# Kernel optimization log

Measured on AMD Instinct MI355X. Metric: run time of the kernel, lower is better.

The kernel has to match this reference:

```python
import jax, jax.numpy as jnp
import numpy as np

N, E = 50000, 800000
IN_DIM, HID, OUT = 64, 128, 64
EPS = 1e-5  # BatchNorm eps


def setup_inputs() -> dict:
    key = jax.random.key(0)
    ks = jax.random.split(key, 16)
    def w(k, i, o):
        return jax.random.normal(k, (i, o), jnp.float32) / np.float32(np.sqrt(i))
    def bn(k):
        km, kv = jax.random.split(k)
        return (jnp.ones((HID,), jnp.float32),                       # gamma
                jnp.zeros((HID,), jnp.float32),                      # beta
                0.1 * jax.random.normal(km, (HID,), jnp.float32),    # running mean
                0.5 + jax.random.uniform(kv, (HID,), jnp.float32))   # running var
    g0, be0, m0, v0 = bn(ks[6])
    g1, be1, m1, v1 = bn(ks[7])
    g2, be2, m2, v2 = bn(ks[8])
    return {
        "x":   jax.random.normal(ks[0], (N, IN_DIM), jnp.float32),
        "src": jax.random.randint(ks[1], (E,), 0, N, jnp.int32),
        "dst": jax.random.randint(ks[2], (E,), 0, N, jnp.int32),
        "W0": w(ks[3], IN_DIM, HID), "b0": jnp.zeros((HID,), jnp.float32),
        "g0": g0, "be0": be0, "m0": m0, "v0": v0,
        "W1": w(ks[4], HID, HID), "b1": jnp.zeros((HID,), jnp.float32),
        "g1": g1, "be1": be1, "m1": m1, "v1": v1,
        "W2": w(ks[5], HID, HID), "b2": jnp.zeros((HID,), jnp.float32),
        "g2": g2, "be2": be2, "m2": m2, "v2": v2,
        "Wm1": w(ks[9], HID, HID), "bm1": jnp.zeros((HID,), jnp.float32),
        "Wm2": w(ks[10], HID, OUT), "bm2": jnp.zeros((OUT,), jnp.float32),
    }


def gcn_conv(x, src, dst, W, b):
    # PyG GCNConv: h = x @ W; add self loops; symmetric normalization; scatter-add; + bias
    h = x @ W                                                     # [N, F]
    ones = jnp.ones((src.shape[0],), h.dtype)
    deg = 1.0 + jax.ops.segment_sum(ones, dst, num_segments=N)   # self loop adds 1
    dinv = jax.lax.rsqrt(deg)                                     # deg^-1/2 (deg >= 1)
    coef = (dinv[src] * dinv[dst])[:, None]                       # per-edge norm
    agg = jax.ops.segment_sum(h[src] * coef, dst, num_segments=N)
    return agg + h * (dinv * dinv)[:, None] + b                   # self-loop term + bias


def bn_relu(x, g, be, m, v):
    # eval-mode BatchNorm1d followed by ReLU (dropout is identity in eval)
    return jax.nn.relu((x - m) * jax.lax.rsqrt(v + EPS) * g + be)


def reference(x, src, dst,
              W0, b0, g0, be0, m0, v0,
              W1, b1, g1, be1, m1, v1,
              W2, b2, g2, be2, m2, v2,
              Wm1, bm1, Wm2, bm2):
    h = bn_relu(gcn_conv(x, src, dst, W0, b0), g0, be0, m0, v0)
    h = bn_relu(gcn_conv(h, src, dst, W1, b1), g1, be1, m1, v1)
    h = bn_relu(gcn_conv(h, src, dst, W2, b2), g2, be2, m2, v2)
    h = jax.nn.relu(h @ Wm1 + bm1)
    return h @ Wm2 + bm2
```

## Files before the change

### kernel.cpp

```cpp
#include <hip/hip_runtime.h>
#include <hip/hip_fp16.h>

#define BN_EPS 1e-5f
#define BK 512
#define NBMAX 128
#define ECH 8192

typedef _Float16 half_t;
typedef _Float16 half8 __attribute__((ext_vector_type(8)));
typedef float floatx4 __attribute__((ext_vector_type(4)));


__global__ void hist_kernel(const int* __restrict__ dst, int* __restrict__ cnt, int E) {
  int e = blockIdx.x * blockDim.x + threadIdx.x;
  if (e < E) atomicAdd(&cnt[dst[e]], 1);
}

__global__ __launch_bounds__(256) void block_sum_kernel(
    const int* __restrict__ cnt, int* __restrict__ bsum, int n) {
  int base = blockIdx.x * 1024 + threadIdx.x * 4;
  int s = 0;
#pragma unroll
  for (int j = 0; j < 4; ++j) {
    int i = base + j;
    if (i < n) s += cnt[i];
  }
#pragma unroll
  for (int o = 32; o > 0; o >>= 1) s += __shfl_down(s, o);
  __shared__ int ws[4];
  int lane = threadIdx.x & 63, w = threadIdx.x >> 6;
  if (lane == 0) ws[w] = s;
  __syncthreads();
  if (threadIdx.x == 0) bsum[blockIdx.x] = ws[0] + ws[1] + ws[2] + ws[3];
}

__global__ void scan_sums_kernel(int* __restrict__ bsum, int nb) {
  int lane = threadIdx.x;
  int v = (lane < nb) ? bsum[lane] : 0;
  int orig = v;
#pragma unroll
  for (int o = 1; o < 64; o <<= 1) {
    int t = __shfl_up(v, o);
    if (lane >= o) v += t;
  }
  if (lane < nb) bsum[lane] = v - orig;
}

__global__ __launch_bounds__(256) void scan_apply_kernel(
    const int* __restrict__ cnt, const int* __restrict__ bsum,
    int* __restrict__ off, float* __restrict__ dinv, int n, int E) {
  __shared__ int ts[256];
  const int t = threadIdx.x;
  const int base = blockIdx.x * 1024 + t * 4;
  int c[4];
  int s = 0;
#pragma unroll
  for (int j = 0; j < 4; ++j) {
    int i = base + j;
    c[j] = (i < n) ? cnt[i] : 0;
    s += c[j];
  }
  ts[t] = s;
  __syncthreads();
  for (int o = 1; o < 256; o <<= 1) {
    int v = (t >= o) ? ts[t - o] : 0;
    __syncthreads();
    ts[t] += v;
    __syncthreads();
  }
  int prefix = bsum[blockIdx.x] + ((t == 0) ? 0 : ts[t - 1]);
#pragma unroll
  for (int j = 0; j < 4; ++j) {
    int i = base + j;
    if (i < n) {
      off[i] = prefix;
      dinv[i] = rsqrtf(1.0f + (float)c[j]);
      prefix += c[j];
    }
  }
  if (blockIdx.x == 0 && t == 0) off[n] = E;
}

__global__ __launch_bounds__(256) void bucket_hist_kernel(
    const int* __restrict__ dst, int* __restrict__ bcnt, int E, int nb) {
  __shared__ int h[NBMAX];
  const int t = threadIdx.x;
  for (int i = t; i < nb; i += 256) h[i] = 0;
  __syncthreads();
  const int base = blockIdx.x * ECH;
#pragma unroll 8
  for (int p = 0; p < ECH / 256; ++p) {
    int e = base + p * 256 + t;
    if (e < E) atomicAdd(&h[dst[e] >> 9], 1);
  }
  __syncthreads();
  for (int i = t; i < nb; i += 256)
    if (h[i]) atomicAdd(&bcnt[i], h[i]);
}

__global__ __launch_bounds__(128) void bucket_scan_kernel(
    const int* __restrict__ bcnt, int* __restrict__ bbase,
    int* __restrict__ bcursor, int nb, int E) {
  __shared__ int ts[128];
  const int t = threadIdx.x;
  int v = (t < nb) ? bcnt[t] : 0;
  ts[t] = v;
  __syncthreads();
  for (int o = 1; o < 128; o <<= 1) {
    int u = (t >= o) ? ts[t - o] : 0;
    __syncthreads();
    ts[t] += u;
    __syncthreads();
  }
  int excl = ts[t] - v;
  if (t < nb) { bbase[t] = excl; bcursor[t] = excl; }
  if (t == 0) bbase[nb] = E;
}

__global__ __launch_bounds__(256) void bucket_scatter_kernel(
    const int* __restrict__ src, const int* __restrict__ dst,
    int* __restrict__ bcursor, int2* __restrict__ tmp, int E, int nb) {
  __shared__ int h[NBMAX];
  const int t = threadIdx.x;
  for (int i = t; i < nb; i += 256) h[i] = 0;
  __syncthreads();
  const int base = blockIdx.x * ECH;
#pragma unroll 8
  for (int p = 0; p < ECH / 256; ++p) {
    int e = base + p * 256 + t;
    if (e < E) atomicAdd(&h[dst[e] >> 9], 1);
  }
  __syncthreads();
  for (int i = t; i < nb; i += 256) {
    int c = h[i];
    h[i] = c ? atomicAdd(&bcursor[i], c) : 0;
  }
  __syncthreads();
#pragma unroll 8
  for (int p = 0; p < ECH / 256; ++p) {
    int e = base + p * 256 + t;
    if (e < E) {
      int s = src[e], d = dst[e];
      int pos = atomicAdd(&h[d >> 9], 1);
      tmp[pos] = make_int2(s, d);
    }
  }
}

__global__ __launch_bounds__(256) void final_scatter_kernel(
    const int2* __restrict__ tmp, const int* __restrict__ bbase,
    const int* __restrict__ off, int* __restrict__ esrc, int n) {
  __shared__ int cur[BK];
  const int t = threadIdx.x;
  const int b = blockIdx.x;
  const int nbase = b * BK;
  const int nn = min(BK, n - nbase);
  for (int i = t; i < nn; i += 256) cur[i] = off[nbase + i];
  __syncthreads();
  const int e0 = bbase[b], e1 = bbase[b + 1];
  for (int e = e0 + t; e < e1; e += 256) {
    int2 r = tmp[e];
    int pos = atomicAdd(&cur[r.y - nbase], 1);
    esrc[pos] = r.x;
  }
}

__global__ void cvt_fp16_kernel(const float* __restrict__ in, __half* __restrict__ out,
                                int n4) {
  int i = blockIdx.x * blockDim.x + threadIdx.x;
  if (i >= n4) return;
  float4 v = *(const float4*)(in + (size_t)i * 4);
  union { __half h[4]; float2 f; } u;
  u.h[0] = __float2half_rn(v.x);
  u.h[1] = __float2half_rn(v.y);
  u.h[2] = __float2half_rn(v.z);
  u.h[3] = __float2half_rn(v.w);
  *(float2*)(out + (size_t)i * 4) = u.f;
}


template <int FIN, int FOUT, int EPI, bool HALFOUT>
__global__ __launch_bounds__(256) void mgemm_kernel(
    const __half* __restrict__ X, const float* __restrict__ W,
    const float* __restrict__ bias, const float* __restrict__ gam,
    const float* __restrict__ bet, const float* __restrict__ mean,
    const float* __restrict__ var, void* __restrict__ Yv, int n) {
  constexpr int LDK = 72;
  constexpr int NCI = FOUT / 16;
  __shared__ half_t Asm[128 * LDK];
  __shared__ half_t Bsm[FOUT * LDK];

  const int t = threadIdx.x;
  const int wave = t >> 6, lane = t & 63;
  const int quad = lane >> 4, l16 = lane & 15;
  const int rowBase = blockIdx.x * 128;

  floatx4 acc[2][NCI];
#pragma unroll
  for (int i = 0; i < 2; ++i)
#pragma unroll
    for (int ci = 0; ci < NCI; ++ci) acc[i][ci] = (floatx4){0.f, 0.f, 0.f, 0.f};

  for (int kc = 0; kc < FIN; kc += 64) {
    __syncthreads();
    {
      const int kq = t & 15, m0 = t >> 4;
#pragma unroll
      for (int p = 0; p < 8; ++p) {
        int m = p * 16 + m0;
        int row = rowBase + m;
        uint2 v = make_uint2(0u, 0u);
        if (row < n) v = *(const uint2*)(X + (size_t)row * FIN + kc + kq * 4);
        *(uint2*)&Asm[m * LDK + kq * 4] = v;
      }
    }
    {
#pragma unroll
      for (int c0 = 0; c0 < FOUT * 16; c0 += 256) {
        int c = c0 + t;
        int nn = c % FOUT;
        int kg = (c / FOUT) * 4;
        const float* wp = W + (size_t)(kc + kg) * FOUT + nn;
        half_t* d = &Bsm[nn * LDK + kg];
        d[0] = (half_t)wp[0];
        d[1] = (half_t)wp[FOUT];
        d[2] = (half_t)wp[2 * FOUT];
        d[3] = (half_t)wp[3 * FOUT];
      }
    }
    __syncthreads();
#pragma unroll
    for (int kk = 0; kk < 2; ++kk) {
      half8 a0 = *(const half8*)&Asm[(wave * 32 + l16) * LDK + kk * 32 + quad * 8];
      half8 a1 = *(const half8*)&Asm[(wave * 32 + 16 + l16) * LDK + kk * 32 + quad * 8];
#pragma unroll
      for (int ci = 0; ci < NCI; ++ci) {
        half8 b = *(const half8*)&Bsm[(ci * 16 + l16) * LDK + kk * 32 + quad * 8];
        acc[0][ci] = __builtin_amdgcn_mfma_f32_16x16x32_f16(a0, b, acc[0][ci], 0, 0, 0);
        acc[1][ci] = __builtin_amdgcn_mfma_f32_16x16x32_f16(a1, b, acc[1][ci], 0, 0, 0);
      }
    }
  }

  float sc[NCI], sh[NCI];
#pragma unroll
  for (int ci = 0; ci < NCI; ++ci) {
    int col = ci * 16 + l16;
    if constexpr (EPI == 3) {
      float s = gam[col] * rsqrtf(var[col] + BN_EPS);
      sc[ci] = s;
      sh[ci] = (bias[col] - mean[col]) * s + bet[col];
    } else if constexpr (EPI == 1 || EPI == 2) {
      sc[ci] = 1.f;
      sh[ci] = bias[col];
    } else {
      sc[ci] = 1.f;
      sh[ci] = 0.f;
    }
  }
#pragma unroll
  for (int ri = 0; ri < 2; ++ri)
#pragma unroll
    for (int ci = 0; ci < NCI; ++ci) {
      int col = ci * 16 + l16;
#pragma unroll
      for (int r = 0; r < 4; ++r) {
        int row = rowBase + wave * 32 + ri * 16 + quad * 4 + r;
        if (row < n) {
          float v = acc[ri][ci][r];
          if constexpr (EPI != 0) v = fmaf(v, sc[ci], sh[ci]);
          if constexpr (EPI == 1 || EPI == 3) v = fmaxf(v, 0.f);
          if constexpr (HALFOUT)
            ((half_t*)Yv)[(size_t)row * FOUT + col] = (half_t)v;
          else
            ((float*)Yv)[(size_t)row * FOUT + col] = v;
        }
      }
    }
}


__global__ __launch_bounds__(256) void agg64_kernel(
    const __half* __restrict__ h, const int* __restrict__ off,
    const int* __restrict__ esrc, const float* __restrict__ dinv,
    __half* __restrict__ out, int n) {
  int gi = blockIdx.x * 4 + (threadIdx.x >> 6);
  if (gi >= n) return;
  const int lane = threadIdx.x & 63;
  const float di = dinv[gi];

  float a = 0.f;
  int e = off[gi];
  const int e1 = off[gi + 1];
  for (; e + 4 <= e1; e += 4) {
    int s0 = esrc[e], s1 = esrc[e + 1], s2 = esrc[e + 2], s3 = esrc[e + 3];
    float h0 = __half2float(h[((size_t)s0 << 6) + lane]);
    float h1 = __half2float(h[((size_t)s1 << 6) + lane]);
    float h2 = __half2float(h[((size_t)s2 << 6) + lane]);
    float h3 = __half2float(h[((size_t)s3 << 6) + lane]);
    a = fmaf(dinv[s0] * di, h0, a);
    a = fmaf(dinv[s1] * di, h1, a);
    a = fmaf(dinv[s2] * di, h2, a);
    a = fmaf(dinv[s3] * di, h3, a);
  }
  for (; e < e1; ++e) {
    int s = esrc[e];
    a = fmaf(dinv[s] * di, __half2float(h[((size_t)s << 6) + lane]), a);
  }
  a = fmaf(di * di, __half2float(h[((size_t)gi << 6) + lane]), a);
  out[((size_t)gi << 6) + lane] = __float2half_rn(a);
}

__global__ __launch_bounds__(256) void agg128_bn_kernel(
    const __half* __restrict__ h, const int* __restrict__ off,
    const int* __restrict__ esrc, const float* __restrict__ dinv,
    const float* __restrict__ bias, const float* __restrict__ gam,
    const float* __restrict__ bet, const float* __restrict__ mean,
    const float* __restrict__ var, __half* __restrict__ out, int n) {
  int gi = blockIdx.x * 4 + (threadIdx.x >> 6);
  if (gi >= n) return;
  const int lane = threadIdx.x & 63;
  const int c = lane << 1;
  const __half2* hp = (const __half2*)h;
  const float di = dinv[gi];

  float ax = 0.f, ay = 0.f;
  int e = off[gi];
  const int e1 = off[gi + 1];
  for (; e + 4 <= e1; e += 4) {
    int s0 = esrc[e], s1 = esrc[e + 1], s2 = esrc[e + 2], s3 = esrc[e + 3];
    float2 h0 = __half22float2(hp[((size_t)s0 << 6) + lane]);
    float2 h1 = __half22float2(hp[((size_t)s1 << 6) + lane]);
    float2 h2 = __half22float2(hp[((size_t)s2 << 6) + lane]);
    float2 h3 = __half22float2(hp[((size_t)s3 << 6) + lane]);
    float c0 = dinv[s0] * di, c1 = dinv[s1] * di;
    float c2 = dinv[s2] * di, c3 = dinv[s3] * di;
    ax = fmaf(c0, h0.x, ax); ay = fmaf(c0, h0.y, ay);
    ax = fmaf(c1, h1.x, ax); ay = fmaf(c1, h1.y, ay);
    ax = fmaf(c2, h2.x, ax); ay = fmaf(c2, h2.y, ay);
    ax = fmaf(c3, h3.x, ax); ay = fmaf(c3, h3.y, ay);
  }
  for (; e < e1; ++e) {
    int s = esrc[e];
    float cf = dinv[s] * di;
    float2 hv = __half22float2(hp[((size_t)s << 6) + lane]);
    ax = fmaf(cf, hv.x, ax);
    ay = fmaf(cf, hv.y, ay);
  }
  float d2 = di * di;
  float2 hs = __half22float2(hp[((size_t)gi << 6) + lane]);
  ax = fmaf(d2, hs.x, ax);
  ay = fmaf(d2, hs.y, ay);

  float2 bv = *(const float2*)(bias + c);
  float2 gv = *(const float2*)(gam + c);
  float2 bev = *(const float2*)(bet + c);
  float2 mv = *(const float2*)(mean + c);
  float2 vv = *(const float2*)(var + c);
  float s0 = gv.x * rsqrtf(vv.x + BN_EPS);
  float s1 = gv.y * rsqrtf(vv.y + BN_EPS);
  float o0 = fmaxf(fmaf(ax + bv.x - mv.x, s0, bev.x), 0.f);
  float o1 = fmaxf(fmaf(ay + bv.y - mv.y, s1, bev.y), 0.f);
  ((__half2*)out)[((size_t)gi << 6) + lane] = __floats2half2_rn(o0, o1);
}


static inline size_t alignup(size_t x, size_t a) { return (x + a - 1) & ~(a - 1); }

extern "C" void kernel_launch(void* const* d_in, const int* in_sizes, int n_in,
                              void* d_out, int out_size, void* d_ws, size_t ws_size,
                              hipStream_t stream) {
  const float* x   = (const float*)d_in[0];
  const int*   src = (const int*)d_in[1];
  const int*   dst = (const int*)d_in[2];
  const float* W0  = (const float*)d_in[3];
  const float* b0  = (const float*)d_in[4];
  const float* g0  = (const float*)d_in[5];
  const float* be0 = (const float*)d_in[6];
  const float* m0  = (const float*)d_in[7];
  const float* v0  = (const float*)d_in[8];
  const float* W1  = (const float*)d_in[9];
  const float* b1  = (const float*)d_in[10];
  const float* g1  = (const float*)d_in[11];
  const float* be1 = (const float*)d_in[12];
  const float* m1  = (const float*)d_in[13];
  const float* v1  = (const float*)d_in[14];
  const float* W2  = (const float*)d_in[15];
  const float* b2  = (const float*)d_in[16];
  const float* g2  = (const float*)d_in[17];
  const float* be2 = (const float*)d_in[18];
  const float* m2  = (const float*)d_in[19];
  const float* v2  = (const float*)d_in[20];
  const float* Wm1 = (const float*)d_in[21];
  const float* bm1 = (const float*)d_in[22];
  const float* Wm2 = (const float*)d_in[23];
  const float* bm2 = (const float*)d_in[24];

  const int N = in_sizes[0] / 64;
  const int E = in_sizes[1];

  char* p = (char*)d_ws;
  auto take = [&](size_t bytes) {
    char* r = p;
    p += alignup(bytes, 256);
    return r;
  };
  int*    cnt    = (int*)take((size_t)(N + NBMAX) * 4);
  int*    bcnt   = cnt + N;
  int*    off    = (int*)take((size_t)(N + 1) * 4);
  float*  dinv   = (float*)take((size_t)N * 4);
  int*    bsum   = (int*)take(64 * 4);
  int*    bbase  = (int*)take((NBMAX + 1) * 4);
  int*    bcursor= (int*)take(NBMAX * 4);
  int*    esrc   = (int*)take((size_t)E * 4);
  int2*   tmp    = (int2*)take((size_t)E * 8);
  __half* x16    = (__half*)take((size_t)N * 64 * 2);
  __half* aggx16 = (__half*)take((size_t)N * 64 * 2);
  __half* t0     = (__half*)take((size_t)N * 128 * 2);
  __half* t1     = (__half*)take((size_t)N * 128 * 2);
  float*  yout   = (float*)d_out;

  const int TB = 256;
  const int nb = (N + 1023) / 1024;
  const int nbk = (N + BK - 1) / BK;
  const int ebk = (E + ECH - 1) / ECH;

  hipMemsetAsync(cnt, 0, (size_t)(N + NBMAX) * 4, stream);
  hist_kernel<<<(E + TB - 1) / TB, TB, 0, stream>>>(dst, cnt, E);
  block_sum_kernel<<<nb, TB, 0, stream>>>(cnt, bsum, N);
  scan_sums_kernel<<<1, 64, 0, stream>>>(bsum, nb);
  scan_apply_kernel<<<nb, TB, 0, stream>>>(cnt, bsum, off, dinv, N, E);
  bucket_hist_kernel<<<ebk, TB, 0, stream>>>(dst, bcnt, E, nbk);
  bucket_scan_kernel<<<1, 128, 0, stream>>>(bcnt, bbase, bcursor, nbk, E);
  bucket_scatter_kernel<<<ebk, TB, 0, stream>>>(src, dst, bcursor, tmp, E, nbk);
  final_scatter_kernel<<<nbk, TB, 0, stream>>>(tmp, bbase, off, esrc, N);
  {
    int n4 = N * 64 / 4;
    cvt_fp16_kernel<<<(n4 + TB - 1) / TB, TB, 0, stream>>>(x, x16, n4);
  }

  const int gemmGrid = (N + 127) / 128;
  const int aggGrid = (N + 3) / 4;

  agg64_kernel<<<aggGrid, TB, 0, stream>>>(x16, off, esrc, dinv, aggx16, N);
  mgemm_kernel<64, 128, 3, true><<<gemmGrid, TB, 0, stream>>>(
      aggx16, W0, b0, g0, be0, m0, v0, t0, N);
  mgemm_kernel<128, 128, 0, true><<<gemmGrid, TB, 0, stream>>>(
      t0, W1, nullptr, nullptr, nullptr, nullptr, nullptr, t1, N);
  agg128_bn_kernel<<<aggGrid, TB, 0, stream>>>(t1, off, esrc, dinv,
                                               b1, g1, be1, m1, v1, t0, N);
  mgemm_kernel<128, 128, 0, true><<<gemmGrid, TB, 0, stream>>>(
      t0, W2, nullptr, nullptr, nullptr, nullptr, nullptr, t1, N);
  agg128_bn_kernel<<<aggGrid, TB, 0, stream>>>(t1, off, esrc, dinv,
                                               b2, g2, be2, m2, v2, t0, N);
  mgemm_kernel<128, 128, 1, true><<<gemmGrid, TB, 0, stream>>>(
      t0, Wm1, bm1, nullptr, nullptr, nullptr, nullptr, t1, N);
  mgemm_kernel<128, 64, 2, false><<<gemmGrid, TB, 0, stream>>>(
      t1, Wm2, bm2, nullptr, nullptr, nullptr, nullptr, yout, N);
}
```

Baseline: 383.2 us.

## Fold degree scan into bucket finalize and fuse the two MLP GEMMs

The separate degree histogram, block-sum, scan and scan-apply kernels are removed. Each destination bucket now counts degrees in shared memory, scans them locally, and writes offsets, dinv and the CSR source list in one kernel. The two head GEMMs are merged into one kernel that keeps the hidden ReLU activations in LDS instead of writing them to global memory and reading them back. This removes several launches and a global atomic histogram pass, at the cost of a larger LDS footprint and serial per-block scans.

```diff
diff --git a/kernel.cpp b/kernel.cpp
--- a/kernel.cpp
+++ b/kernel.cpp
@@ -10,76 +10,6 @@
 typedef _Float16 half8 __attribute__((ext_vector_type(8)));
 typedef float floatx4 __attribute__((ext_vector_type(4)));
 
-
-__global__ void hist_kernel(const int* __restrict__ dst, int* __restrict__ cnt, int E) {
-  int e = blockIdx.x * blockDim.x + threadIdx.x;
-  if (e < E) atomicAdd(&cnt[dst[e]], 1);
-}
-
-__global__ __launch_bounds__(256) void block_sum_kernel(
-    const int* __restrict__ cnt, int* __restrict__ bsum, int n) {
-  int base = blockIdx.x * 1024 + threadIdx.x * 4;
-  int s = 0;
-#pragma unroll
-  for (int j = 0; j < 4; ++j) {
-    int i = base + j;
-    if (i < n) s += cnt[i];
-  }
-#pragma unroll
-  for (int o = 32; o > 0; o >>= 1) s += __shfl_down(s, o);
-  __shared__ int ws[4];
-  int lane = threadIdx.x & 63, w = threadIdx.x >> 6;
-  if (lane == 0) ws[w] = s;
-  __syncthreads();
-  if (threadIdx.x == 0) bsum[blockIdx.x] = ws[0] + ws[1] + ws[2] + ws[3];
-}
-
-__global__ void scan_sums_kernel(int* __restrict__ bsum, int nb) {
-  int lane = threadIdx.x;
-  int v = (lane < nb) ? bsum[lane] : 0;
-  int orig = v;
-#pragma unroll
-  for (int o = 1; o < 64; o <<= 1) {
-    int t = __shfl_up(v, o);
-    if (lane >= o) v += t;
-  }
-  if (lane < nb) bsum[lane] = v - orig;
-}
-
-__global__ __launch_bounds__(256) void scan_apply_kernel(
-    const int* __restrict__ cnt, const int* __restrict__ bsum,
-    int* __restrict__ off, float* __restrict__ dinv, int n, int E) {
-  __shared__ int ts[256];
-  const int t = threadIdx.x;
-  const int base = blockIdx.x * 1024 + t * 4;
-  int c[4];
-  int s = 0;
-#pragma unroll
-  for (int j = 0; j < 4; ++j) {
-    int i = base + j;
-    c[j] = (i < n) ? cnt[i] : 0;
-    s += c[j];
-  }
-  ts[t] = s;
-  __syncthreads();
-  for (int o = 1; o < 256; o <<= 1) {
-    int v = (t >= o) ? ts[t - o] : 0;
-    __syncthreads();
-    ts[t] += v;
-    __syncthreads();
-  }
-  int prefix = bsum[blockIdx.x] + ((t == 0) ? 0 : ts[t - 1]);
-#pragma unroll
-  for (int j = 0; j < 4; ++j) {
-    int i = base + j;
-    if (i < n) {
-      off[i] = prefix;
-      dinv[i] = rsqrtf(1.0f + (float)c[j]);
-      prefix += c[j];
-    }
-  }
-  if (blockIdx.x == 0 && t == 0) off[n] = E;
-}
 
 __global__ __launch_bounds__(256) void bucket_hist_kernel(
     const int* __restrict__ dst, int* __restrict__ bcnt, int E, int nb) {
@@ -147,22 +77,51 @@
   }
 }
 
-__global__ __launch_bounds__(256) void final_scatter_kernel(
+__global__ __launch_bounds__(256) void bucket_finalize_kernel(
     const int2* __restrict__ tmp, const int* __restrict__ bbase,
-    const int* __restrict__ off, int* __restrict__ esrc, int n) {
+    int* __restrict__ off, float* __restrict__ dinv,
+    int* __restrict__ esrc, int n, int E) {
+  __shared__ int deg[BK];
   __shared__ int cur[BK];
+  __shared__ int ts[256];
   const int t = threadIdx.x;
   const int b = blockIdx.x;
   const int nbase = b * BK;
   const int nn = min(BK, n - nbase);
-  for (int i = t; i < nn; i += 256) cur[i] = off[nbase + i];
+  for (int i = t; i < nn; i += 256) deg[i] = 0;
   __syncthreads();
   const int e0 = bbase[b], e1 = bbase[b + 1];
+  for (int e = e0 + t; e < e1; e += 256)
+    atomicAdd(&deg[tmp[e].y - nbase], 1);
+  __syncthreads();
+  int d0 = (2 * t < nn) ? deg[2 * t] : 0;
+  int d1 = (2 * t + 1 < nn) ? deg[2 * t + 1] : 0;
+  ts[t] = d0 + d1;
+  __syncthreads();
+  for (int o = 1; o < 256; o <<= 1) {
+    int v = (t >= o) ? ts[t - o] : 0;
+    __syncthreads();
+    ts[t] += v;
+    __syncthreads();
+  }
+  int base = e0 + ((t == 0) ? 0 : ts[t - 1]);
+  if (2 * t < nn) {
+    off[nbase + 2 * t] = base;
+    cur[2 * t] = base;
+    dinv[nbase + 2 * t] = rsqrtf(1.0f + (float)d0);
+  }
+  if (2 * t + 1 < nn) {
+    off[nbase + 2 * t + 1] = base + d0;
+    cur[2 * t + 1] = base + d0;
+    dinv[nbase + 2 * t + 1] = rsqrtf(1.0f + (float)d1);
+  }
+  __syncthreads();
   for (int e = e0 + t; e < e1; e += 256) {
     int2 r = tmp[e];
     int pos = atomicAdd(&cur[r.y - nbase], 1);
     esrc[pos] = r.x;
   }
+  if (b == 0 && t == 0) off[n] = E;
 }
 
 __global__ void cvt_fp16_kernel(const float* __restrict__ in, __half* __restrict__ out,
@@ -275,6 +234,130 @@
           else
             ((float*)Yv)[(size_t)row * FOUT + col] = v;
         }
+      }
+    }
+}
+
+
+__global__ __launch_bounds__(256) void mlp_kernel(
+    const __half* __restrict__ X, const float* __restrict__ W1,
+    const float* __restrict__ b1f, const float* __restrict__ W2,
+    const float* __restrict__ b2f, float* __restrict__ Y, int n) {
+  constexpr int LDK = 72;
+  constexpr int LDK2 = 136;
+  __shared__ half_t smem[(128 + 64) * LDK2];
+  half_t* As1 = smem;
+  half_t* Bs1 = smem + 128 * LDK;
+  half_t* As2 = smem;
+  half_t* Bs2 = smem + 128 * LDK2;
+
+  const int t = threadIdx.x;
+  const int wave = t >> 6, lane = t & 63;
+  const int quad = lane >> 4, l16 = lane & 15;
+  const int rowBase = blockIdx.x * 128;
+
+  floatx4 acc[2][8];
+#pragma unroll
+  for (int i = 0; i < 2; ++i)
+#pragma unroll
+    for (int ci = 0; ci < 8; ++ci) acc[i][ci] = (floatx4){0.f, 0.f, 0.f, 0.f};
+
+  for (int kc = 0; kc < 128; kc += 64) {
+    __syncthreads();
+    {
+      const int kq = t & 15, m0 = t >> 4;
+#pragma unroll
+      for (int p = 0; p < 8; ++p) {
+        int m = p * 16 + m0;
+        int row = rowBase + m;
+        uint2 v = make_uint2(0u, 0u);
+        if (row < n) v = *(const uint2*)(X + (size_t)row * 128 + kc + kq * 4);
+        *(uint2*)&As1[m * LDK + kq * 4] = v;
+      }
+    }
+    {
+#pragma unroll
+      for (int c0 = 0; c0 < 128 * 16; c0 += 256) {
+        int c = c0 + t;
+        int nn = c & 127;
+        int kg = (c >> 7) << 2;
+        const float* wp = W1 + (size_t)(kc + kg) * 128 + nn;
+        half_t* d = &Bs1[nn * LDK + kg];
+        d[0] = (half_t)wp[0];
+        d[1] = (half_t)wp[128];
+        d[2] = (half_t)wp[256];
+        d[3] = (half_t)wp[384];
+      }
+    }
+    __syncthreads();
+#pragma unroll
+    for (int kk = 0; kk < 2; ++kk) {
+      half8 a0 = *(const half8*)&As1[(wave * 32 + l16) * LDK + kk * 32 + quad * 8];
+      half8 a1 = *(const half8*)&As1[(wave * 32 + 16 + l16) * LDK + kk * 32 + quad * 8];
+#pragma unroll
+      for (int ci = 0; ci < 8; ++ci) {
+        half8 b = *(const half8*)&Bs1[(ci * 16 + l16) * LDK + kk * 32 + quad * 8];
+        acc[0][ci] = __builtin_amdgcn_mfma_f32_16x16x32_f16(a0, b, acc[0][ci], 0, 0, 0);
+        acc[1][ci] = __builtin_amdgcn_mfma_f32_16x16x32_f16(a1, b, acc[1][ci], 0, 0, 0);
+      }
+    }
+  }
+  __syncthreads();
+
+#pragma unroll
+  for (int ri = 0; ri < 2; ++ri)
+#pragma unroll
+    for (int ci = 0; ci < 8; ++ci) {
+      int col = ci * 16 + l16;
+      float bz = b1f[col];
+#pragma unroll
+      for (int r = 0; r < 4; ++r) {
+        int m = wave * 32 + ri * 16 + quad * 4 + r;
+        As2[m * LDK2 + col] = (half_t)fmaxf(acc[ri][ci][r] + bz, 0.f);
+      }
+    }
+  {
+#pragma unroll
+    for (int c0 = 0; c0 < 64 * 32; c0 += 256) {
+      int c = c0 + t;
+      int nn = c & 63;
+      int kg = (c >> 6) << 2;
+      const float* wp = W2 + (size_t)kg * 64 + nn;
+      half_t* d = &Bs2[nn * LDK2 + kg];
+      d[0] = (half_t)wp[0];
+      d[1] = (half_t)wp[64];
+      d[2] = (half_t)wp[128];
+      d[3] = (half_t)wp[192];
+    }
+  }
+  __syncthreads();
+
+  floatx4 acc2[2][4];
+#pragma unroll
+  for (int i = 0; i < 2; ++i)
+#pragma unroll
+    for (int ci = 0; ci < 4; ++ci) acc2[i][ci] = (floatx4){0.f, 0.f, 0.f, 0.f};
+#pragma unroll
+  for (int kk = 0; kk < 4; ++kk) {
+    half8 a0 = *(const half8*)&As2[(wave * 32 + l16) * LDK2 + kk * 32 + quad * 8];
+    half8 a1 = *(const half8*)&As2[(wave * 32 + 16 + l16) * LDK2 + kk * 32 + quad * 8];
+#pragma unroll
+    for (int ci = 0; ci < 4; ++ci) {
+      half8 b = *(const half8*)&Bs2[(ci * 16 + l16) * LDK2 + kk * 32 + quad * 8];
+      acc2[0][ci] = __builtin_amdgcn_mfma_f32_16x16x32_f16(a0, b, acc2[0][ci], 0, 0, 0);
+      acc2[1][ci] = __builtin_amdgcn_mfma_f32_16x16x32_f16(a1, b, acc2[1][ci], 0, 0, 0);
+    }
+  }
+#pragma unroll
+  for (int ri = 0; ri < 2; ++ri)
+#pragma unroll
+    for (int ci = 0; ci < 4; ++ci) {
+      int col = ci * 16 + l16;
+      float bz = b2f[col];
+#pragma unroll
+      for (int r = 0; r < 4; ++r) {
+        int row = rowBase + wave * 32 + ri * 16 + quad * 4 + r;
+        if (row < n) Y[(size_t)row * 64 + col] = acc2[ri][ci][r] + bz;
       }
     }
 }
@@ -405,13 +488,11 @@
     p += alignup(bytes, 256);
     return r;
   };
-  int*    cnt    = (int*)take((size_t)(N + NBMAX) * 4);
-  int*    bcnt   = cnt + N;
+  int*    bcnt   = (int*)take(NBMAX * 4);
+  int*    bbase  = (int*)take((NBMAX + 1) * 4);
+  int*    bcursor= (int*)take(NBMAX * 4);
   int*    off    = (int*)take((size_t)(N + 1) * 4);
   float*  dinv   = (float*)take((size_t)N * 4);
-  int*    bsum   = (int*)take(64 * 4);
-  int*    bbase  = (int*)take((NBMAX + 1) * 4);
-  int*    bcursor= (int*)take(NBMAX * 4);
   int*    esrc   = (int*)take((size_t)E * 4);
   int2*   tmp    = (int2*)take((size_t)E * 8);
   __half* x16    = (__half*)take((size_t)N * 64 * 2);
@@ -421,19 +502,14 @@
   float*  yout   = (float*)d_out;
 
   const int TB = 256;
-  const int nb = (N + 1023) / 1024;
   const int nbk = (N + BK - 1) / BK;
   const int ebk = (E + ECH - 1) / ECH;
 
-  hipMemsetAsync(cnt, 0, (size_t)(N + NBMAX) * 4, stream);
-  hist_kernel<<<(E + TB - 1) / TB, TB, 0, stream>>>(dst, cnt, E);
-  block_sum_kernel<<<nb, TB, 0, stream>>>(cnt, bsum, N);
-  scan_sums_kernel<<<1, 64, 0, stream>>>(bsum, nb);
-  scan_apply_kernel<<<nb, TB, 0, stream>>>(cnt, bsum, off, dinv, N, E);
+  hipMemsetAsync(bcnt, 0, NBMAX * 4, stream);
   bucket_hist_kernel<<<ebk, TB, 0, stream>>>(dst, bcnt, E, nbk);
   bucket_scan_kernel<<<1, 128, 0, stream>>>(bcnt, bbase, bcursor, nbk, E);
   bucket_scatter_kernel<<<ebk, TB, 0, stream>>>(src, dst, bcursor, tmp, E, nbk);
-  final_scatter_kernel<<<nbk, TB, 0, stream>>>(tmp, bbase, off, esrc, N);
+  bucket_finalize_kernel<<<nbk, TB, 0, stream>>>(tmp, bbase, off, dinv, esrc, N, E);
   {
     int n4 = N * 64 / 4;
     cvt_fp16_kernel<<<(n4 + TB - 1) / TB, TB, 0, stream>>>(x, x16, n4);
@@ -453,8 +529,5 @@
       t0, W2, nullptr, nullptr, nullptr, nullptr, nullptr, t1, N);
   agg128_bn_kernel<<<aggGrid, TB, 0, stream>>>(t1, off, esrc, dinv,
                                                b2, g2, be2, m2, v2, t0, N);
-  mgemm_kernel<128, 128, 1, true><<<gemmGrid, TB, 0, stream>>>(
-      t0, Wm1, bm1, nullptr, nullptr, nullptr, nullptr, t1, N);
-  mgemm_kernel<128, 64, 2, false><<<gemmGrid, TB, 0, stream>>>(
-      t1, Wm2, bm2, nullptr, nullptr, nullptr, nullptr, yout, N);
-}
+  mlp_kernel<<<gemmGrid, TB, 0, stream>>>(t0, Wm1, bm1, Wm2, bm2, yout, N);
+}
```

New measurement: 338.3 us. -11.7%, faster.
